# Kernel tuning notes

Measured on AMD Instinct MI355X. Metric: run time of the kernel, lower is better.

Reference implementation:

```python
import jax, jax.numpy as jnp
import numpy as np

DIM = 128
HEADS = 4


def setup_inputs() -> dict:
    key = jax.random.key(0)
    ks = jax.random.split(key, 6)
    B_, N, C = 2048, 49, DIM
    nW = 64
    x = jax.random.normal(ks[0], (B_, N, C), dtype=jnp.float32)
    mask = jax.random.normal(ks[1], (nW, N, N), dtype=jnp.float32)
    qkv_w = jax.random.normal(ks[2], (3 * C, C), dtype=jnp.float32) * 0.02
    qkv_b = jnp.zeros((3 * C,), dtype=jnp.float32)
    proj_w = jax.random.normal(ks[3], (C, C), dtype=jnp.float32) * 0.02
    proj_b = jnp.zeros((C,), dtype=jnp.float32)
    return {"x": x, "mask": mask, "qkv_w": qkv_w, "qkv_b": qkv_b,
            "proj_w": proj_w, "proj_b": proj_b}


def reference(x, mask, qkv_w, qkv_b, proj_w, proj_b):
    B_, N, C = x.shape
    H = HEADS
    Dh = C // H
    scale = Dh ** (-0.5)
    # fused QKV projection: [B_, N, 3C]
    qkv = x @ qkv_w.T + qkv_b
    qkv = qkv.reshape(B_, N, 3, H, Dh).transpose(2, 0, 3, 1, 4)  # [3, B_, H, N, Dh]
    q, k, v = qkv[0] * scale, qkv[1], qkv[2]
    attn = jnp.einsum('bhqd,bhkd->bhqk', q, k)  # [B_, H, N, N]
    nW = mask.shape[0]
    # add per-window additive mask: broadcast over images and heads
    attn = attn.reshape(B_ // nW, nW, H, N, N) + mask[None, :, None, :, :]
    attn = jax.nn.softmax(attn.reshape(B_, H, N, N), axis=-1)
    out = jnp.einsum('bhqk,bhkd->bhqd', attn, v)  # [B_, H, N, Dh]
    out = out.transpose(0, 2, 1, 3).reshape(B_, N, C)
    return out @ proj_w.T + proj_b
```

## Files before the change

kernel.cpp:

```cpp
#include <hip/hip_runtime.h>

typedef __bf16 bf16_t;
typedef __bf16 bf16x2 __attribute__((ext_vector_type(2)));
typedef __bf16 bf16x4 __attribute__((ext_vector_type(4)));
typedef __bf16 bf16x8 __attribute__((ext_vector_type(8)));
typedef float  f32x4  __attribute__((ext_vector_type(4)));
typedef float  f32x4u __attribute__((ext_vector_type(4), aligned(4)));
typedef unsigned int u32;

#define MFMA16(a, b, c) __builtin_amdgcn_mfma_f32_16x16x32_bf16((a), (b), (c), 0, 0, 0)

#define ROWB 272


union W8 { u32 u[4]; bf16x8 v; };

__device__ __forceinline__ u32 pack2(float a, float b) {
    union { bf16x2 h; u32 u; } c;
    c.h[0] = (bf16_t)a; c.h[1] = (bf16_t)b;
    return c.u;
}

__device__ __forceinline__ void st4(char* base, int row, int byteoff, bf16x4 v) {
    *(bf16x4*)(base + row * ROWB + byteoff) = v;
}
__device__ __forceinline__ bf16x8 ld8(const char* base, int row, int byteoff) {
    return *(const bf16x8*)(base + row * ROWB + byteoff);
}

__device__ __forceinline__ bf16x8 redist4(u32 w0, u32 w1, u32 w2, u32 w3,
                                          bool gl, bool gh) {
    u32 wd[4] = {w0, w1, w2, w3};
    u32 X[4], Y[4], Z[4];
    #pragma unroll
    for (int j = 0; j < 4; ++j) X[j] = __shfl_xor(wd[j], 16);
    #pragma unroll
    for (int j = 0; j < 4; ++j) Y[j] = __shfl_xor(wd[j], 32);
    #pragma unroll
    for (int j = 0; j < 4; ++j) Z[j] = __shfl_xor(X[j], 32);
    W8 u;
    #pragma unroll
    for (int t = 0; t < 4; ++t) {
        int j0 = t & 1;
        int j1 = j0 + 2;
        u32 lo, hi;
        if (t < 2) { lo = gl ? Z[j0] : wd[j0]; hi = gl ? X[j1] : Y[j1]; }
        else       { lo = gl ? Y[j0] : X[j0];  hi = gl ? wd[j1] : Z[j1]; }
        u.u[t] = gh ? hi : lo;
    }
    return u.v;
}

__global__ void wconv_kernel(const float* __restrict__ qw, const float* __restrict__ pw,
                             bf16_t* __restrict__ o) {
    int i = (blockIdx.x * 256 + threadIdx.x) * 4;
    const float* src = (i < 49152) ? (qw + i) : (pw + (i - 49152));
    float4 f = *(const float4*)src;
    bf16x4 h;
    h[0] = (bf16_t)f.x; h[1] = (bf16_t)f.y; h[2] = (bf16_t)f.z; h[3] = (bf16_t)f.w;
    *(bf16x4*)(o + i) = h;
}

template<int USEB>
__device__ __forceinline__ bf16x8 ldw(const float* __restrict__ wf,
                                      const bf16_t* __restrict__ wb, int idx) {
    if constexpr (USEB) {
        return *(const bf16x8*)(wb + idx);
    } else {
        float4 f0 = *(const float4*)(wf + idx);
        float4 f1 = *(const float4*)(wf + idx + 4);
        bf16x8 r;
        r[0] = (bf16_t)f0.x; r[1] = (bf16_t)f0.y; r[2] = (bf16_t)f0.z; r[3] = (bf16_t)f0.w;
        r[4] = (bf16_t)f1.x; r[5] = (bf16_t)f1.y; r[6] = (bf16_t)f1.z; r[7] = (bf16_t)f1.w;
        return r;
    }
}

template<int USEB>
__device__ __forceinline__ void pass_rowmajor(
    const char* xs, const float* __restrict__ wf, const bf16_t* __restrict__ wb,
    int rowbase, const float* __restrict__ biasp, float scale,
    int g, int c0, bool gl, bool gh, bf16x8 out[4])
{
    f32x4 acc[2][4];
    #pragma unroll
    for (int d = 0; d < 2; ++d)
        #pragma unroll
        for (int mt = 0; mt < 4; ++mt) acc[d][mt] = {0.f, 0.f, 0.f, 0.f};
    #pragma unroll
    for (int ks = 0; ks < 4; ++ks) {
        bf16x8 w0 = ldw<USEB>(wf, wb, (rowbase + c0) * 128 + 32 * ks + 8 * g);
        bf16x8 w1 = ldw<USEB>(wf, wb, (rowbase + 16 + c0) * 128 + 32 * ks + 8 * g);
        #pragma unroll
        for (int mt = 0; mt < 4; ++mt) {
            bf16x8 xf = ld8(xs, 16 * mt + c0, (32 * ks + 8 * g) * 2);
            acc[0][mt] = MFMA16(w0, xf, acc[0][mt]);
            acc[1][mt] = MFMA16(w1, xf, acc[1][mt]);
        }
    }
    float4 b0 = *(const float4*)(biasp + rowbase + 4 * g);
    float4 b1 = *(const float4*)(biasp + rowbase + 16 + 4 * g);
    #pragma unroll
    for (int t = 0; t < 4; ++t) {
        out[t] = redist4(
            pack2((acc[0][t][0] + b0.x) * scale, (acc[0][t][1] + b0.y) * scale),
            pack2((acc[0][t][2] + b0.z) * scale, (acc[0][t][3] + b0.w) * scale),
            pack2((acc[1][t][0] + b1.x) * scale, (acc[1][t][1] + b1.y) * scale),
            pack2((acc[1][t][2] + b1.z) * scale, (acc[1][t][3] + b1.w) * scale),
            gl, gh);
    }
}

template<int USEB>
__global__ __launch_bounds__(256, 4) void winattn_kernel(
    const float* __restrict__ xg, const float* __restrict__ maskg,
    const float* __restrict__ qwg, const float* __restrict__ qbg,
    const float* __restrict__ pwg, const float* __restrict__ pbg,
    const bf16_t* __restrict__ wqb, const bf16_t* __restrict__ wpb,
    const int nW, float* __restrict__ outg)
{
    __shared__ char xs[17408];

    const int b    = blockIdx.x;
    const int tid  = threadIdx.x;
    const int w    = tid >> 6;
    const int lane = tid & 63;
    const int g    = lane >> 4;
    const int c0   = lane & 15;
    const bool gl  = (g & 1) != 0, gh = (g & 2) != 0;
    const int h    = w;

    {
        const float4* xb = (const float4*)(xg + (long)b * 6272);
        #pragma unroll
        for (int it = 0; it < 7; ++it) {
            int i = tid + it * 256;
            if (i < 1568) {
                float4 f = xb[i];
                int row = i >> 5, colb = (i & 31) << 3;
                bf16x4 hq;
                hq[0] = (bf16_t)f.x; hq[1] = (bf16_t)f.y; hq[2] = (bf16_t)f.z; hq[3] = (bf16_t)f.w;
                st4(xs, row, colb, hq);
            }
        }
        #pragma unroll
        for (int it = 0; it < 4; ++it) {
            int i = tid + it * 256;
            if (i < 960) {
                int row = 49 + (i >> 6), byteo = (i & 63) << 2;
                *(u32*)(xs + row * ROWB + byteo) = 0u;
            }
        }
    }
    __syncthreads();

    const float qs = 0.17677669529663687f;
    bf16x8 qfr[4], ka[4];
    pass_rowmajor<USEB>(xs, qwg, wqb, 32 * h,       qbg, qs,  g, c0, gl, gh, qfr);
    pass_rowmajor<USEB>(xs, qwg, wqb, 128 + 32 * h, qbg, 1.f, g, c0, gl, gh, ka);

    bf16x8 va[2][2];
    {
        const int rb = 256 + 32 * h;
        f32x4 acc[4][2];
        #pragma unroll
        for (int mt = 0; mt < 4; ++mt)
            #pragma unroll
            for (int d = 0; d < 2; ++d) acc[mt][d] = {0.f, 0.f, 0.f, 0.f};
        #pragma unroll
        for (int ks = 0; ks < 4; ++ks) {
            bf16x8 w0 = ldw<USEB>(qwg, wqb, (rb + c0) * 128 + 32 * ks + 8 * g);
            bf16x8 w1 = ldw<USEB>(qwg, wqb, (rb + 16 + c0) * 128 + 32 * ks + 8 * g);
            #pragma unroll
            for (int mt = 0; mt < 4; ++mt) {
                bf16x8 xf = ld8(xs, 16 * mt + c0, (32 * ks + 8 * g) * 2);
                acc[mt][0] = MFMA16(xf, w0, acc[mt][0]);
                acc[mt][1] = MFMA16(xf, w1, acc[mt][1]);
            }
        }
        float vb0 = qbg[rb + c0];
        float vb1 = qbg[rb + 16 + c0];
        #pragma unroll
        for (int kt = 0; kt < 2; ++kt) {
            va[0][kt] = redist4(
                pack2(acc[2 * kt][0][0] + vb0, acc[2 * kt][0][1] + vb0),
                pack2(acc[2 * kt][0][2] + vb0, acc[2 * kt][0][3] + vb0),
                pack2(acc[2 * kt + 1][0][0] + vb0, acc[2 * kt + 1][0][1] + vb0),
                pack2(acc[2 * kt + 1][0][2] + vb0, acc[2 * kt + 1][0][3] + vb0),
                gl, gh);
            va[1][kt] = redist4(
                pack2(acc[2 * kt][1][0] + vb1, acc[2 * kt][1][1] + vb1),
                pack2(acc[2 * kt][1][2] + vb1, acc[2 * kt][1][3] + vb1),
                pack2(acc[2 * kt + 1][1][0] + vb1, acc[2 * kt + 1][1][1] + vb1),
                pack2(acc[2 * kt + 1][1][2] + vb1, acc[2 * kt + 1][1][3] + vb1),
                gl, gh);
        }
    }
    __syncthreads();

    const float* mrow = maskg + (long)(b % nW) * 2401;
    #pragma unroll
    for (int nt = 0; nt < 4; ++nt) {
        f32x4 s[4];
        #pragma unroll
        for (int kt = 0; kt < 4; ++kt) s[kt] = {0.f, 0.f, 0.f, 0.f};
        #pragma unroll
        for (int kt = 0; kt < 4; ++kt)
            s[kt] = MFMA16(ka[kt], qfr[nt], s[kt]);

        {
            int q  = 16 * nt + c0;
            int qm = q < 49 ? q : 48;
            const float* mr = mrow + qm * 49;
            f32x4u m0 = *(const f32x4u*)(mr + 4 * g);
            f32x4u m1 = *(const f32x4u*)(mr + 16 + 4 * g);
            f32x4u m2 = *(const f32x4u*)(mr + 32 + 4 * g);
            float m48 = mr[48];
            #pragma unroll
            for (int r = 0; r < 4; ++r) {
                s[0][r] += m0[r]; s[1][r] += m1[r]; s[2][r] += m2[r];
            }
            s[3][0] = (g == 0) ? s[3][0] + m48 : -1e30f;
            s[3][1] = -1e30f; s[3][2] = -1e30f; s[3][3] = -1e30f;
        }

        float mx = -1e30f;
        #pragma unroll
        for (int kt = 0; kt < 4; ++kt)
            #pragma unroll
            for (int r = 0; r < 4; ++r) mx = fmaxf(mx, s[kt][r]);
        mx = fmaxf(mx, __shfl_xor(mx, 16));
        mx = fmaxf(mx, __shfl_xor(mx, 32));

        float sum = 0.f;
        u32 wd[8];
        #pragma unroll
        for (int kt = 0; kt < 4; ++kt) {
            float e0 = __expf(s[kt][0] - mx), e1 = __expf(s[kt][1] - mx);
            float e2 = __expf(s[kt][2] - mx), e3 = __expf(s[kt][3] - mx);
            sum += (e0 + e1) + (e2 + e3);
            wd[2 * kt]     = pack2(e0, e1);
            wd[2 * kt + 1] = pack2(e2, e3);
        }
        sum += __shfl_xor(sum, 16);
        sum += __shfl_xor(sum, 32);
        float inv = 1.f / sum;

        bf16x8 pa0 = redist4(wd[0], wd[1], wd[2], wd[3], gl, gh);
        bf16x8 pa1 = redist4(wd[4], wd[5], wd[6], wd[7], gl, gh);

        f32x4 oo[2];
        oo[0] = {0.f, 0.f, 0.f, 0.f}; oo[1] = {0.f, 0.f, 0.f, 0.f};
        oo[0] = MFMA16(va[0][0], pa0, oo[0]);
        oo[0] = MFMA16(va[0][1], pa1, oo[0]);
        oo[1] = MFMA16(va[1][0], pa0, oo[1]);
        oo[1] = MFMA16(va[1][1], pa1, oo[1]);

        int q = 16 * nt + c0;
        #pragma unroll
        for (int dt = 0; dt < 2; ++dt) {
            bf16x4 t;
            t[0] = (bf16_t)(oo[dt][0] * inv); t[1] = (bf16_t)(oo[dt][1] * inv);
            t[2] = (bf16_t)(oo[dt][2] * inv); t[3] = (bf16_t)(oo[dt][3] * inv);
            st4(xs, q, (32 * h + 16 * dt + 4 * g) * 2, t);
        }
    }
    __syncthreads();

    {
        f32x4 acc[2][4];
        #pragma unroll
        for (int nt = 0; nt < 2; ++nt)
            #pragma unroll
            for (int mt = 0; mt < 4; ++mt) acc[nt][mt] = {0.f, 0.f, 0.f, 0.f};
        #pragma unroll
        for (int ks = 0; ks < 4; ++ks) {
            bf16x8 p0 = ldw<USEB>(pwg, wpb, (32 * w + c0) * 128 + 32 * ks + 8 * g);
            bf16x8 p1 = ldw<USEB>(pwg, wpb, (32 * w + 16 + c0) * 128 + 32 * ks + 8 * g);
            #pragma unroll
            for (int mt = 0; mt < 4; ++mt) {
                bf16x8 af = ld8(xs, 16 * mt + c0, (32 * ks + 8 * g) * 2);
                acc[0][mt] = MFMA16(p0, af, acc[0][mt]);
                acc[1][mt] = MFMA16(p1, af, acc[1][mt]);
            }
        }
        float4 pb0 = *(const float4*)(pbg + 32 * w + 4 * g);
        float4 pb1 = *(const float4*)(pbg + 32 * w + 16 + 4 * g);
        float* ob = outg + (long)b * 6272;
        #pragma unroll
        for (int nt = 0; nt < 2; ++nt) {
            float4 pb = nt ? pb1 : pb0;
            #pragma unroll
            for (int mt = 0; mt < 4; ++mt) {
                int tok = 16 * mt + c0;
                if (tok < 49) {
                    float4 t;
                    t.x = acc[nt][mt][0] + pb.x;
                    t.y = acc[nt][mt][1] + pb.y;
                    t.z = acc[nt][mt][2] + pb.z;
                    t.w = acc[nt][mt][3] + pb.w;
                    *(float4*)(ob + tok * 128 + 32 * w + 16 * nt + 4 * g) = t;
                }
            }
        }
    }
}

extern "C" void kernel_launch(void* const* d_in, const int* in_sizes, int n_in,
                              void* d_out, int out_size, void* d_ws, size_t ws_size,
                              hipStream_t stream) {
    const float* xg  = (const float*)d_in[0];
    const float* mg  = (const float*)d_in[1];
    const float* qwg = (const float*)d_in[2];
    const float* qbg = (const float*)d_in[3];
    const float* pwg = (const float*)d_in[4];
    const float* pbg = (const float*)d_in[5];
    float* outg = (float*)d_out;

    const int B  = in_sizes[0] / (49 * 128);
    const int nW = in_sizes[1] / (49 * 49);

    int use_wbf = (d_ws != nullptr && ws_size >= 131072) ? 1 : 0;
    bf16_t* wqb = (bf16_t*)d_ws;
    bf16_t* wpb = use_wbf ? (wqb + 49152) : nullptr;

    if (use_wbf) {
        wconv_kernel<<<64, 256, 0, stream>>>(qwg, pwg, wqb);
        winattn_kernel<1><<<B, 256, 0, stream>>>(
            xg, mg, qwg, qbg, pwg, pbg, wqb, wpb, nW, outg);
    } else {
        winattn_kernel<0><<<B, 256, 0, stream>>>(
            xg, mg, qwg, qbg, pwg, pbg, nullptr, nullptr, nW, outg);
    }
}
```

Baseline: 67.36 us.

## Load x fragments directly into registers, drop LDS staging and syncs

Each wave now reads its x rows straight from global memory into bf16 register fragments instead of staging the whole window through shared memory. This removes the LDS store/load round trip and two barriers. The projection weights and bias are also prefetched before the final barrier. In exchange every wave reloads all of x (four times the global/L2 traffic), register pressure rises, and launch bounds drop from four blocks per CU to three, reducing occupancy.

```diff
diff --git a/kernel.cpp b/kernel.cpp
--- a/kernel.cpp
+++ b/kernel.cpp
@@ -77,8 +77,8 @@
 }
 
 template<int USEB>
-__device__ __forceinline__ void pass_rowmajor(
-    const char* xs, const float* __restrict__ wf, const bf16_t* __restrict__ wb,
+__device__ __forceinline__ void qk_pass(
+    const bf16x8 xf[4][4], const float* __restrict__ wf, const bf16_t* __restrict__ wb,
     int rowbase, const float* __restrict__ biasp, float scale,
     int g, int c0, bool gl, bool gh, bf16x8 out[4])
 {
@@ -93,9 +93,8 @@
         bf16x8 w1 = ldw<USEB>(wf, wb, (rowbase + 16 + c0) * 128 + 32 * ks + 8 * g);
         #pragma unroll
         for (int mt = 0; mt < 4; ++mt) {
-            bf16x8 xf = ld8(xs, 16 * mt + c0, (32 * ks + 8 * g) * 2);
-            acc[0][mt] = MFMA16(w0, xf, acc[0][mt]);
-            acc[1][mt] = MFMA16(w1, xf, acc[1][mt]);
+            acc[0][mt] = MFMA16(w0, xf[mt][ks], acc[0][mt]);
+            acc[1][mt] = MFMA16(w1, xf[mt][ks], acc[1][mt]);
         }
     }
     float4 b0 = *(const float4*)(biasp + rowbase + 4 * g);
@@ -112,14 +111,14 @@
 }
 
 template<int USEB>
-__global__ __launch_bounds__(256, 4) void winattn_kernel(
+__global__ __launch_bounds__(256, 3) void winattn_kernel(
     const float* __restrict__ xg, const float* __restrict__ maskg,
     const float* __restrict__ qwg, const float* __restrict__ qbg,
     const float* __restrict__ pwg, const float* __restrict__ pbg,
     const bf16_t* __restrict__ wqb, const bf16_t* __restrict__ wpb,
     const int nW, float* __restrict__ outg)
 {
-    __shared__ char xs[17408];
+    __shared__ char as_[17408];
 
     const int b    = blockIdx.x;
     const int tid  = threadIdx.x;
@@ -130,34 +129,30 @@
     const bool gl  = (g & 1) != 0, gh = (g & 2) != 0;
     const int h    = w;
 
+    bf16x8 xf[4][4];
     {
-        const float4* xb = (const float4*)(xg + (long)b * 6272);
-        #pragma unroll
-        for (int it = 0; it < 7; ++it) {
-            int i = tid + it * 256;
-            if (i < 1568) {
-                float4 f = xb[i];
-                int row = i >> 5, colb = (i & 31) << 3;
-                bf16x4 hq;
-                hq[0] = (bf16_t)f.x; hq[1] = (bf16_t)f.y; hq[2] = (bf16_t)f.z; hq[3] = (bf16_t)f.w;
-                st4(xs, row, colb, hq);
-            }
-        }
-        #pragma unroll
-        for (int it = 0; it < 4; ++it) {
-            int i = tid + it * 256;
-            if (i < 960) {
-                int row = 49 + (i >> 6), byteo = (i & 63) << 2;
-                *(u32*)(xs + row * ROWB + byteo) = 0u;
-            }
-        }
-    }
-    __syncthreads();
+        const float* xb = xg + (long)b * 6272;
+        #pragma unroll
+        for (int mt = 0; mt < 4; ++mt) {
+            int row = 16 * mt + c0;
+            row = row > 48 ? 48 : row;
+            const float* rp = xb + row * 128 + 8 * g;
+            #pragma unroll
+            for (int ks = 0; ks < 4; ++ks) {
+                float4 f0 = *(const float4*)(rp + 32 * ks);
+                float4 f1 = *(const float4*)(rp + 32 * ks + 4);
+                bf16x8 r;
+                r[0] = (bf16_t)f0.x; r[1] = (bf16_t)f0.y; r[2] = (bf16_t)f0.z; r[3] = (bf16_t)f0.w;
+                r[4] = (bf16_t)f1.x; r[5] = (bf16_t)f1.y; r[6] = (bf16_t)f1.z; r[7] = (bf16_t)f1.w;
+                xf[mt][ks] = r;
+            }
+        }
+    }
 
     const float qs = 0.17677669529663687f;
     bf16x8 qfr[4], ka[4];
-    pass_rowmajor<USEB>(xs, qwg, wqb, 32 * h,       qbg, qs,  g, c0, gl, gh, qfr);
-    pass_rowmajor<USEB>(xs, qwg, wqb, 128 + 32 * h, qbg, 1.f, g, c0, gl, gh, ka);
+    qk_pass<USEB>(xf, qwg, wqb, 32 * h,       qbg, qs,  g, c0, gl, gh, qfr);
+    qk_pass<USEB>(xf, qwg, wqb, 128 + 32 * h, qbg, 1.f, g, c0, gl, gh, ka);
 
     bf16x8 va[2][2];
     {
@@ -173,9 +168,8 @@
             bf16x8 w1 = ldw<USEB>(qwg, wqb, (rb + 16 + c0) * 128 + 32 * ks + 8 * g);
             #pragma unroll
             for (int mt = 0; mt < 4; ++mt) {
-                bf16x8 xf = ld8(xs, 16 * mt + c0, (32 * ks + 8 * g) * 2);
-                acc[mt][0] = MFMA16(xf, w0, acc[mt][0]);
-                acc[mt][1] = MFMA16(xf, w1, acc[mt][1]);
+                acc[mt][0] = MFMA16(xf[mt][ks], w0, acc[mt][0]);
+                acc[mt][1] = MFMA16(xf[mt][ks], w1, acc[mt][1]);
             }
         }
         float vb0 = qbg[rb + c0];
@@ -196,7 +190,6 @@
                 gl, gh);
         }
     }
-    __syncthreads();
 
     const float* mrow = maskg + (long)(b % nW) * 2401;
     #pragma unroll
@@ -262,9 +255,18 @@
             bf16x4 t;
             t[0] = (bf16_t)(oo[dt][0] * inv); t[1] = (bf16_t)(oo[dt][1] * inv);
             t[2] = (bf16_t)(oo[dt][2] * inv); t[3] = (bf16_t)(oo[dt][3] * inv);
-            st4(xs, q, (32 * h + 16 * dt + 4 * g) * 2, t);
-        }
-    }
+            st4(as_, q, (32 * h + 16 * dt + 4 * g) * 2, t);
+        }
+    }
+
+    bf16x8 pwf[4][2];
+    #pragma unroll
+    for (int ks = 0; ks < 4; ++ks) {
+        pwf[ks][0] = ldw<USEB>(pwg, wpb, (32 * w + c0) * 128 + 32 * ks + 8 * g);
+        pwf[ks][1] = ldw<USEB>(pwg, wpb, (32 * w + 16 + c0) * 128 + 32 * ks + 8 * g);
+    }
+    float4 pb0 = *(const float4*)(pbg + 32 * w + 4 * g);
+    float4 pb1 = *(const float4*)(pbg + 32 * w + 16 + 4 * g);
     __syncthreads();
 
     {
@@ -275,17 +277,13 @@
             for (int mt = 0; mt < 4; ++mt) acc[nt][mt] = {0.f, 0.f, 0.f, 0.f};
         #pragma unroll
         for (int ks = 0; ks < 4; ++ks) {
-            bf16x8 p0 = ldw<USEB>(pwg, wpb, (32 * w + c0) * 128 + 32 * ks + 8 * g);
-            bf16x8 p1 = ldw<USEB>(pwg, wpb, (32 * w + 16 + c0) * 128 + 32 * ks + 8 * g);
             #pragma unroll
             for (int mt = 0; mt < 4; ++mt) {
-                bf16x8 af = ld8(xs, 16 * mt + c0, (32 * ks + 8 * g) * 2);
-                acc[0][mt] = MFMA16(p0, af, acc[0][mt]);
-                acc[1][mt] = MFMA16(p1, af, acc[1][mt]);
-            }
-        }
-        float4 pb0 = *(const float4*)(pbg + 32 * w + 4 * g);
-        float4 pb1 = *(const float4*)(pbg + 32 * w + 16 + 4 * g);
+                bf16x8 af = ld8(as_, 16 * mt + c0, (32 * ks + 8 * g) * 2);
+                acc[0][mt] = MFMA16(pwf[ks][0], af, acc[0][mt]);
+                acc[1][mt] = MFMA16(pwf[ks][1], af, acc[1][mt]);
+            }
+        }
         float* ob = outg + (long)b * 6272;
         #pragma unroll
         for (int nt = 0; nt < 2; ++nt) {
```

New measurement: 87.55 us. 30.0% more time.

## Split fused window attention into QKV projection and attention kernels

Applied to the files above, without the earlier changes.

Adds a two-kernel path: one kernel computes the QKV projection per window and writes bf16 Q/K/V to workspace in per-head layouts, and a second kernel reads them, runs masked softmax attention and the output projection. Each projection kernel spreads all 384 output channels across the four waves, which aims to balance MFMA work and cut the per-block register and serial-phase cost of the monolithic kernel. The split adds a round trip through global memory for Q/K/V (about 100 MB for B=2048) and one extra launch. It also hoists the projection weight loads before the barrier in both the fused and split attention paths.

```diff
diff --git a/kernel.cpp b/kernel.cpp
--- a/kernel.cpp
+++ b/kernel.cpp
@@ -76,8 +76,262 @@
     }
 }
 
+
 template<int USEB>
-__device__ __forceinline__ void pass_rowmajor(
+__global__ __launch_bounds__(256, 4) void qkv_kernel(
+    const float* __restrict__ xg, const float* __restrict__ qwg,
+    const float* __restrict__ qbg, const bf16_t* __restrict__ wqb,
+    bf16_t* __restrict__ qkv)
+{
+    __shared__ char xs[17408];
+    const int b    = blockIdx.x;
+    const int tid  = threadIdx.x;
+    const int w    = tid >> 6;
+    const int lane = tid & 63;
+    const int g    = lane >> 4;
+    const int c0   = lane & 15;
+
+    {
+        const float4* xb = (const float4*)(xg + (long)b * 6272);
+        #pragma unroll
+        for (int it = 0; it < 7; ++it) {
+            int i = tid + it * 256;
+            if (i < 1568) {
+                float4 f = xb[i];
+                int row = i >> 5, colb = (i & 31) << 3;
+                bf16x4 hq;
+                hq[0] = (bf16_t)f.x; hq[1] = (bf16_t)f.y; hq[2] = (bf16_t)f.z; hq[3] = (bf16_t)f.w;
+                st4(xs, row, colb, hq);
+            }
+        }
+        #pragma unroll
+        for (int it = 0; it < 4; ++it) {
+            int i = tid + it * 256;
+            if (i < 960) {
+                int row = 49 + (i >> 6), byteo = (i & 63) << 2;
+                *(u32*)(xs + row * ROWB + byteo) = 0u;
+            }
+        }
+    }
+    __syncthreads();
+
+    bf16_t* wb = qkv + (long)b * 24576;
+    const float qs = 0.17677669529663687f;
+
+    #pragma unroll
+    for (int half = 0; half < 2; ++half) {
+        f32x4 acc[3][4];
+        #pragma unroll
+        for (int t = 0; t < 3; ++t)
+            #pragma unroll
+            for (int mt = 0; mt < 4; ++mt) acc[t][mt] = {0.f, 0.f, 0.f, 0.f};
+
+        const int jb = 3 * half;
+        #pragma unroll
+        for (int ks = 0; ks < 4; ++ks) {
+            bf16x8 wf[3];
+            #pragma unroll
+            for (int t = 0; t < 3; ++t) {
+                int o0 = 96 * w + 16 * (jb + t);
+                wf[t] = ldw<USEB>(qwg, wqb, (o0 + c0) * 128 + 32 * ks + 8 * g);
+            }
+            #pragma unroll
+            for (int mt = 0; mt < 4; ++mt) {
+                bf16x8 xfm = ld8(xs, 16 * mt + c0, (32 * ks + 8 * g) * 2);
+                #pragma unroll
+                for (int t = 0; t < 3; ++t) {
+                    int o0 = 96 * w + 16 * (jb + t);
+                    if (o0 < 256) acc[t][mt] = MFMA16(wf[t], xfm, acc[t][mt]);
+                    else          acc[t][mt] = MFMA16(xfm, wf[t], acc[t][mt]);
+                }
+            }
+        }
+        #pragma unroll
+        for (int t = 0; t < 3; ++t) {
+            int o0   = 96 * w + 16 * (jb + t);
+            int part = o0 >> 7;
+            int hh   = (o0 >> 5) & 3;
+            bf16_t* hb = wb + hh * 6144;
+            if (part < 2) {
+                float4 b4 = *(const float4*)(qbg + o0 + 4 * g);
+                float sc  = (part == 0) ? qs : 1.f;
+                bf16_t* dst = hb + (part == 0 ? 0 : 2048);
+                int dh0 = (o0 & 31) + 4 * g;
+                #pragma unroll
+                for (int mt = 0; mt < 4; ++mt) {
+                    int tok = 16 * mt + c0;
+                    bf16x4 tv;
+                    tv[0] = (bf16_t)((acc[t][mt][0] + b4.x) * sc);
+                    tv[1] = (bf16_t)((acc[t][mt][1] + b4.y) * sc);
+                    tv[2] = (bf16_t)((acc[t][mt][2] + b4.z) * sc);
+                    tv[3] = (bf16_t)((acc[t][mt][3] + b4.w) * sc);
+                    *(bf16x4*)(dst + tok * 32 + dh0) = tv;
+                }
+            } else {
+                float bv = qbg[o0 + c0];
+                bf16_t* dst = hb + 4096;
+                int dh = (o0 & 31) + c0;
+                #pragma unroll
+                for (int mt = 0; mt < 4; ++mt) {
+                    bf16x4 tv;
+                    tv[0] = (bf16_t)(acc[t][mt][0] + bv);
+                    tv[1] = (bf16_t)(acc[t][mt][1] + bv);
+                    tv[2] = (bf16_t)(acc[t][mt][2] + bv);
+                    tv[3] = (bf16_t)(acc[t][mt][3] + bv);
+                    *(bf16x4*)(dst + dh * 64 + 16 * mt + 4 * g) = tv;
+                }
+            }
+        }
+    }
+}
+
+template<int USEB>
+__global__ __launch_bounds__(256, 4) void attn_kernel(
+    const bf16_t* __restrict__ qkv, const float* __restrict__ maskg,
+    const float* __restrict__ pwg, const float* __restrict__ pbg,
+    const bf16_t* __restrict__ wpb, const int nW, float* __restrict__ outg)
+{
+    __shared__ char as_[17408];
+
+    const int b    = blockIdx.x;
+    const int tid  = threadIdx.x;
+    const int w    = tid >> 6;
+    const int lane = tid & 63;
+    const int g    = lane >> 4;
+    const int c0   = lane & 15;
+    const bool gl  = (g & 1) != 0, gh = (g & 2) != 0;
+    const int h    = w;
+
+    const bf16_t* hb = qkv + (long)b * 24576 + h * 6144;
+    bf16x8 qfr[4], ka[4], va[2][2];
+    #pragma unroll
+    for (int t = 0; t < 4; ++t)
+        qfr[t] = *(const bf16x8*)(hb + (16 * t + c0) * 32 + 8 * g);
+    #pragma unroll
+    for (int kt = 0; kt < 4; ++kt)
+        ka[kt] = *(const bf16x8*)(hb + 2048 + (16 * kt + c0) * 32 + 8 * g);
+    #pragma unroll
+    for (int fi = 0; fi < 2; ++fi)
+        #pragma unroll
+        for (int kt = 0; kt < 2; ++kt)
+            va[fi][kt] = *(const bf16x8*)(hb + 4096 + (16 * fi + c0) * 64 + 32 * kt + 8 * g);
+
+    const float* mrow = maskg + (long)(b % nW) * 2401;
+    #pragma unroll
+    for (int nt = 0; nt < 4; ++nt) {
+        f32x4 s[4];
+        #pragma unroll
+        for (int kt = 0; kt < 4; ++kt) s[kt] = {0.f, 0.f, 0.f, 0.f};
+        #pragma unroll
+        for (int kt = 0; kt < 4; ++kt)
+            s[kt] = MFMA16(ka[kt], qfr[nt], s[kt]);
+
+        {
+            int q  = 16 * nt + c0;
+            int qm = q < 49 ? q : 48;
+            const float* mr = mrow + qm * 49;
+            f32x4u m0 = *(const f32x4u*)(mr + 4 * g);
+            f32x4u m1 = *(const f32x4u*)(mr + 16 + 4 * g);
+            f32x4u m2 = *(const f32x4u*)(mr + 32 + 4 * g);
+            float m48 = mr[48];
+            #pragma unroll
+            for (int r = 0; r < 4; ++r) {
+                s[0][r] += m0[r]; s[1][r] += m1[r]; s[2][r] += m2[r];
+            }
+            s[3][0] = (g == 0) ? s[3][0] + m48 : -1e30f;
+            s[3][1] = -1e30f; s[3][2] = -1e30f; s[3][3] = -1e30f;
+        }
+
+        float mx = -1e30f;
+        #pragma unroll
+        for (int kt = 0; kt < 4; ++kt)
+            #pragma unroll
+            for (int r = 0; r < 4; ++r) mx = fmaxf(mx, s[kt][r]);
+        mx = fmaxf(mx, __shfl_xor(mx, 16));
+        mx = fmaxf(mx, __shfl_xor(mx, 32));
+
+        float sum = 0.f;
+        u32 wd[8];
+        #pragma unroll
+        for (int kt = 0; kt < 4; ++kt) {
+            float e0 = __expf(s[kt][0] - mx), e1 = __expf(s[kt][1] - mx);
+            float e2 = __expf(s[kt][2] - mx), e3 = __expf(s[kt][3] - mx);
+            sum += (e0 + e1) + (e2 + e3);
+            wd[2 * kt]     = pack2(e0, e1);
+            wd[2 * kt + 1] = pack2(e2, e3);
+        }
+        sum += __shfl_xor(sum, 16);
+        sum += __shfl_xor(sum, 32);
+        float inv = 1.f / sum;
+
+        bf16x8 pa0 = redist4(wd[0], wd[1], wd[2], wd[3], gl, gh);
+        bf16x8 pa1 = redist4(wd[4], wd[5], wd[6], wd[7], gl, gh);
+
+        f32x4 oo[2];
+        oo[0] = {0.f, 0.f, 0.f, 0.f}; oo[1] = {0.f, 0.f, 0.f, 0.f};
+        oo[0] = MFMA16(va[0][0], pa0, oo[0]);
+        oo[0] = MFMA16(va[0][1], pa1, oo[0]);
+        oo[1] = MFMA16(va[1][0], pa0, oo[1]);
+        oo[1] = MFMA16(va[1][1], pa1, oo[1]);
+
+        int q = 16 * nt + c0;
+        #pragma unroll
+        for (int dt = 0; dt < 2; ++dt) {
+            bf16x4 t;
+            t[0] = (bf16_t)(oo[dt][0] * inv); t[1] = (bf16_t)(oo[dt][1] * inv);
+            t[2] = (bf16_t)(oo[dt][2] * inv); t[3] = (bf16_t)(oo[dt][3] * inv);
+            st4(as_, q, (32 * h + 16 * dt + 4 * g) * 2, t);
+        }
+    }
+
+    bf16x8 pwf[4][2];
+    #pragma unroll
+    for (int ks = 0; ks < 4; ++ks) {
+        pwf[ks][0] = ldw<USEB>(pwg, wpb, (32 * w + c0) * 128 + 32 * ks + 8 * g);
+        pwf[ks][1] = ldw<USEB>(pwg, wpb, (32 * w + 16 + c0) * 128 + 32 * ks + 8 * g);
+    }
+    float4 pb0 = *(const float4*)(pbg + 32 * w + 4 * g);
+    float4 pb1 = *(const float4*)(pbg + 32 * w + 16 + 4 * g);
+    __syncthreads();
+
+    {
+        f32x4 acc[2][4];
+        #pragma unroll
+        for (int nt = 0; nt < 2; ++nt)
+            #pragma unroll
+            for (int mt = 0; mt < 4; ++mt) acc[nt][mt] = {0.f, 0.f, 0.f, 0.f};
+        #pragma unroll
+        for (int ks = 0; ks < 4; ++ks) {
+            #pragma unroll
+            for (int mt = 0; mt < 4; ++mt) {
+                bf16x8 af = ld8(as_, 16 * mt + c0, (32 * ks + 8 * g) * 2);
+                acc[0][mt] = MFMA16(pwf[ks][0], af, acc[0][mt]);
+                acc[1][mt] = MFMA16(pwf[ks][1], af, acc[1][mt]);
+            }
+        }
+        float* ob = outg + (long)b * 6272;
+        #pragma unroll
+        for (int nt = 0; nt < 2; ++nt) {
+            float4 pb = nt ? pb1 : pb0;
+            #pragma unroll
+            for (int mt = 0; mt < 4; ++mt) {
+                int tok = 16 * mt + c0;
+                if (tok < 49) {
+                    float4 t;
+                    t.x = acc[nt][mt][0] + pb.x;
+                    t.y = acc[nt][mt][1] + pb.y;
+                    t.z = acc[nt][mt][2] + pb.z;
+                    t.w = acc[nt][mt][3] + pb.w;
+                    *(float4*)(ob + tok * 128 + 32 * w + 16 * nt + 4 * g) = t;
+                }
+            }
+        }
+    }
+}
+
+
+template<int USEB>
+__device__ __forceinline__ void qk_pass_f(
     const char* xs, const float* __restrict__ wf, const bf16_t* __restrict__ wb,
     int rowbase, const float* __restrict__ biasp, float scale,
     int g, int c0, bool gl, bool gh, bf16x8 out[4])
@@ -156,8 +410,8 @@
 
     const float qs = 0.17677669529663687f;
     bf16x8 qfr[4], ka[4];
-    pass_rowmajor<USEB>(xs, qwg, wqb, 32 * h,       qbg, qs,  g, c0, gl, gh, qfr);
-    pass_rowmajor<USEB>(xs, qwg, wqb, 128 + 32 * h, qbg, 1.f, g, c0, gl, gh, ka);
+    qk_pass_f<USEB>(xs, qwg, wqb, 32 * h,       qbg, qs,  g, c0, gl, gh, qfr);
+    qk_pass_f<USEB>(xs, qwg, wqb, 128 + 32 * h, qbg, 1.f, g, c0, gl, gh, ka);
 
     bf16x8 va[2][2];
     {
@@ -265,6 +519,15 @@
             st4(xs, q, (32 * h + 16 * dt + 4 * g) * 2, t);
         }
     }
+
+    bf16x8 pwf[4][2];
+    #pragma unroll
+    for (int ks = 0; ks < 4; ++ks) {
+        pwf[ks][0] = ldw<USEB>(pwg, wpb, (32 * w + c0) * 128 + 32 * ks + 8 * g);
+        pwf[ks][1] = ldw<USEB>(pwg, wpb, (32 * w + 16 + c0) * 128 + 32 * ks + 8 * g);
+    }
+    float4 pb0 = *(const float4*)(pbg + 32 * w + 4 * g);
+    float4 pb1 = *(const float4*)(pbg + 32 * w + 16 + 4 * g);
     __syncthreads();
 
     {
@@ -275,17 +538,13 @@
             for (int mt = 0; mt < 4; ++mt) acc[nt][mt] = {0.f, 0.f, 0.f, 0.f};
         #pragma unroll
         for (int ks = 0; ks < 4; ++ks) {
-            bf16x8 p0 = ldw<USEB>(pwg, wpb, (32 * w + c0) * 128 + 32 * ks + 8 * g);
-            bf16x8 p1 = ldw<USEB>(pwg, wpb, (32 * w + 16 + c0) * 128 + 32 * ks + 8 * g);
             #pragma unroll
             for (int mt = 0; mt < 4; ++mt) {
                 bf16x8 af = ld8(xs, 16 * mt + c0, (32 * ks + 8 * g) * 2);
-                acc[0][mt] = MFMA16(p0, af, acc[0][mt]);
-                acc[1][mt] = MFMA16(p1, af, acc[1][mt]);
-            }
-        }
-        float4 pb0 = *(const float4*)(pbg + 32 * w + 4 * g);
-        float4 pb1 = *(const float4*)(pbg + 32 * w + 16 + 4 * g);
+                acc[0][mt] = MFMA16(pwf[ks][0], af, acc[0][mt]);
+                acc[1][mt] = MFMA16(pwf[ks][1], af, acc[1][mt]);
+            }
+        }
         float* ob = outg + (long)b * 6272;
         #pragma unroll
         for (int nt = 0; nt < 2; ++nt) {
@@ -320,11 +579,19 @@
     const int B  = in_sizes[0] / (49 * 128);
     const int nW = in_sizes[1] / (49 * 49);
 
-    int use_wbf = (d_ws != nullptr && ws_size >= 131072) ? 1 : 0;
-    bf16_t* wqb = (bf16_t*)d_ws;
-    bf16_t* wpb = use_wbf ? (wqb + 49152) : nullptr;
-
-    if (use_wbf) {
+    const size_t QKV_EL    = (size_t)B * 24576;
+    const size_t NEED_SPLIT = QKV_EL * 2 + 131072;
+
+    if (d_ws != nullptr && ws_size >= NEED_SPLIT) {
+        bf16_t* qkvws = (bf16_t*)d_ws;
+        bf16_t* wqb   = qkvws + QKV_EL;
+        bf16_t* wpb   = wqb + 49152;
+        wconv_kernel<<<64, 256, 0, stream>>>(qwg, pwg, wqb);
+        qkv_kernel<1><<<B, 256, 0, stream>>>(xg, qwg, qbg, wqb, qkvws);
+        attn_kernel<1><<<B, 256, 0, stream>>>(qkvws, mg, pwg, pbg, wpb, nW, outg);
+    } else if (d_ws != nullptr && ws_size >= 131072) {
+        bf16_t* wqb = (bf16_t*)d_ws;
+        bf16_t* wpb = wqb + 49152;
         wconv_kernel<<<64, 256, 0, stream>>>(qwg, pwg, wqb);
         winattn_kernel<1><<<B, 256, 0, stream>>>(
             xg, mg, qwg, qbg, pwg, pbg, wqb, wpb, nW, outg);
```

Result: slower. 129.9 us (+92.8%).

## Persistent multi-window blocks with register-resident QKV weights and x prefetch

Applied to the files above, without the earlier changes.

Replaces the one-window-per-block kernel with a persistent 512-thread kernel where each of 512 blocks handles B/512 windows in sequence. Each wave keeps its QK weight fragments in registers across windows, and the work is split among 8 waves, with Q/K/V staged in dynamic shared memory per head. The next window's x is prefetched into registers during attention. The goal is to avoid reloading weights per window and to hide global load latency, at the cost of more barriers per window, 75KB of LDS, and only 512 blocks for occupancy.

```diff
diff --git a/kernel.cpp b/kernel.cpp
--- a/kernel.cpp
+++ b/kernel.cpp
@@ -26,6 +26,11 @@
 }
 __device__ __forceinline__ bf16x8 ld8(const char* base, int row, int byteoff) {
     return *(const bf16x8*)(base + row * ROWB + byteoff);
+}
+__device__ __forceinline__ void stx(char* buf, int i, float4 f) {
+    bf16x4 hq;
+    hq[0] = (bf16_t)f.x; hq[1] = (bf16_t)f.y; hq[2] = (bf16_t)f.z; hq[3] = (bf16_t)f.w;
+    st4(buf, i >> 5, (i & 31) << 3, hq);
 }
 
 __device__ __forceinline__ bf16x8 redist4(u32 w0, u32 w1, u32 w2, u32 w3,
@@ -61,24 +66,253 @@
     *(bf16x4*)(o + i) = h;
 }
 
-template<int USEB>
-__device__ __forceinline__ bf16x8 ldw(const float* __restrict__ wf,
-                                      const bf16_t* __restrict__ wb, int idx) {
-    if constexpr (USEB) {
-        return *(const bf16x8*)(wb + idx);
-    } else {
-        float4 f0 = *(const float4*)(wf + idx);
-        float4 f1 = *(const float4*)(wf + idx + 4);
-        bf16x8 r;
-        r[0] = (bf16_t)f0.x; r[1] = (bf16_t)f0.y; r[2] = (bf16_t)f0.z; r[3] = (bf16_t)f0.w;
-        r[4] = (bf16_t)f1.x; r[5] = (bf16_t)f1.y; r[6] = (bf16_t)f1.z; r[7] = (bf16_t)f1.w;
-        return r;
-    }
-}
-
-template<int USEB>
-__device__ __forceinline__ void pass_rowmajor(
-    const char* xs, const float* __restrict__ wf, const bf16_t* __restrict__ wb,
+__global__ __launch_bounds__(512, 4) void mwin_kernel(
+    const float* __restrict__ xg, const float* __restrict__ maskg,
+    const bf16_t* __restrict__ wqb, const float* __restrict__ qbg,
+    const bf16_t* __restrict__ wpb, const float* __restrict__ pbg,
+    const int nW, const int WPB, const int Btot, float* __restrict__ outg)
+{
+    extern __shared__ char smem[];
+    char*   xbuf  = smem;
+    bf16_t* heads = (bf16_t*)(smem + 17408);
+
+    const int tid  = threadIdx.x;
+    const int w    = tid >> 6;
+    const int lane = tid & 63;
+    const int g    = lane >> 4;
+    const int c0   = lane & 15;
+    const bool gl  = (g & 1) != 0, gh = (g & 2) != 0;
+    const float qs = 0.17677669529663687f;
+
+    const int oqk = 32 * w;
+    bf16x8 wqk[2][4];
+    #pragma unroll
+    for (int nt = 0; nt < 2; ++nt)
+        #pragma unroll
+        for (int ks = 0; ks < 4; ++ks)
+            wqk[nt][ks] = *(const bf16x8*)(wqb + (oqk + 16*nt + c0)*128 + 32*ks + 8*g);
+    float4 bqk[2];
+    bqk[0] = *(const float4*)(qbg + oqk + 4*g);
+    bqk[1] = *(const float4*)(qbg + oqk + 16 + 4*g);
+    const int   ov   = 256 + 16 * w;
+    const float bv   = qbg[ov + c0];
+    const float qmul = (w < 4) ? qs : 1.f;
+
+    bf16_t* qkdst = heads + (w & 3) * 7424 + (w < 4 ? 0 : 2560);
+    bf16_t* vdst  = heads + (w >> 1) * 7424 + 5120 + (16*(w & 1) + c0) * 72;
+
+    const int h = w >> 1, qh2 = w & 1;
+    const bf16_t* qls = heads + h * 7424;
+    const bf16_t* kls = qls + 2560;
+    const bf16_t* vls = qls + 5120;
+
+    const long b0 = (long)blockIdx.x * WPB;
+    if (b0 >= Btot) return;
+
+    for (int i = tid; i < 960; i += 512) {
+        int row = 49 + (i >> 6), byteo = (i & 63) << 2;
+        *(u32*)(xbuf + row * ROWB + byteo) = 0u;
+    }
+    {
+        const float4* xb = (const float4*)(xg + b0 * 6272);
+        float4 f0 = xb[tid], f1 = xb[tid + 512], f2 = xb[tid + 1024];
+        stx(xbuf, tid, f0); stx(xbuf, tid + 512, f1); stx(xbuf, tid + 1024, f2);
+        if (tid < 32) { float4 f3 = xb[tid + 1536]; stx(xbuf, tid + 1536, f3); }
+    }
+    __syncthreads();
+
+    for (int j = 0; j < WPB; ++j) {
+        const long b = b0 + j;
+
+        {
+            f32x4 aqk[2][4];
+            #pragma unroll
+            for (int nt = 0; nt < 2; ++nt)
+                #pragma unroll
+                for (int mt = 0; mt < 4; ++mt) aqk[nt][mt] = {0.f, 0.f, 0.f, 0.f};
+            #pragma unroll
+            for (int ks = 0; ks < 4; ++ks)
+                #pragma unroll
+                for (int mt = 0; mt < 4; ++mt) {
+                    bf16x8 xf = ld8(xbuf, 16*mt + c0, (32*ks + 8*g) * 2);
+                    aqk[0][mt] = MFMA16(wqk[0][ks], xf, aqk[0][mt]);
+                    aqk[1][mt] = MFMA16(wqk[1][ks], xf, aqk[1][mt]);
+                }
+            #pragma unroll
+            for (int nt = 0; nt < 2; ++nt) {
+                int dh0 = 16*nt + 4*g;
+                #pragma unroll
+                for (int mt = 0; mt < 4; ++mt) {
+                    int tok = 16*mt + c0;
+                    bf16x4 tv;
+                    tv[0] = (bf16_t)((aqk[nt][mt][0] + bqk[nt].x) * qmul);
+                    tv[1] = (bf16_t)((aqk[nt][mt][1] + bqk[nt].y) * qmul);
+                    tv[2] = (bf16_t)((aqk[nt][mt][2] + bqk[nt].z) * qmul);
+                    tv[3] = (bf16_t)((aqk[nt][mt][3] + bqk[nt].w) * qmul);
+                    *(bf16x4*)(qkdst + tok*40 + dh0) = tv;
+                }
+            }
+            f32x4 av[4];
+            #pragma unroll
+            for (int mt = 0; mt < 4; ++mt) av[mt] = {0.f, 0.f, 0.f, 0.f};
+            #pragma unroll
+            for (int ks = 0; ks < 4; ++ks) {
+                bf16x8 wvk = *(const bf16x8*)(wqb + (ov + c0)*128 + 32*ks + 8*g);
+                #pragma unroll
+                for (int mt = 0; mt < 4; ++mt) {
+                    bf16x8 xf = ld8(xbuf, 16*mt + c0, (32*ks + 8*g) * 2);
+                    av[mt] = MFMA16(xf, wvk, av[mt]);
+                }
+            }
+            #pragma unroll
+            for (int mt = 0; mt < 4; ++mt) {
+                bf16x4 tv;
+                tv[0] = (bf16_t)(av[mt][0] + bv);
+                tv[1] = (bf16_t)(av[mt][1] + bv);
+                tv[2] = (bf16_t)(av[mt][2] + bv);
+                tv[3] = (bf16_t)(av[mt][3] + bv);
+                *(bf16x4*)(vdst + 16*mt + 4*g) = tv;
+            }
+        }
+        __syncthreads();
+
+        float4 xr0, xr1, xr2, xr3;
+        const bool pre = (j + 1 < WPB);
+        if (pre) {
+            const float4* xn = (const float4*)(xg + (b + 1) * 6272);
+            xr0 = xn[tid]; xr1 = xn[tid + 512]; xr2 = xn[tid + 1024];
+            if (tid < 32) xr3 = xn[tid + 1536];
+        }
+        {
+            bf16x8 ka[4], qb2[2], va[2][2];
+            #pragma unroll
+            for (int kt = 0; kt < 4; ++kt)
+                ka[kt] = *(const bf16x8*)(kls + (16*kt + c0)*40 + 8*g);
+            #pragma unroll
+            for (int nt = 0; nt < 2; ++nt)
+                qb2[nt] = *(const bf16x8*)(qls + ((2*qh2 + nt)*16 + c0)*40 + 8*g);
+            #pragma unroll
+            for (int fi = 0; fi < 2; ++fi)
+                #pragma unroll
+                for (int kt = 0; kt < 2; ++kt)
+                    va[fi][kt] = *(const bf16x8*)(vls + (16*fi + c0)*72 + 32*kt + 8*g);
+
+            const float* mrow = maskg + (long)(b % nW) * 2401;
+            #pragma unroll
+            for (int nt = 0; nt < 2; ++nt) {
+                f32x4 s[4];
+                #pragma unroll
+                for (int kt = 0; kt < 4; ++kt) s[kt] = {0.f, 0.f, 0.f, 0.f};
+                #pragma unroll
+                for (int kt = 0; kt < 4; ++kt)
+                    s[kt] = MFMA16(ka[kt], qb2[nt], s[kt]);
+
+                int q  = (2*qh2 + nt)*16 + c0;
+                int qm = q < 49 ? q : 48;
+                const float* mr = mrow + qm * 49;
+                f32x4u m0 = *(const f32x4u*)(mr + 4*g);
+                f32x4u m1 = *(const f32x4u*)(mr + 16 + 4*g);
+                f32x4u m2 = *(const f32x4u*)(mr + 32 + 4*g);
+                float m48 = mr[48];
+                #pragma unroll
+                for (int r = 0; r < 4; ++r) {
+                    s[0][r] += m0[r]; s[1][r] += m1[r]; s[2][r] += m2[r];
+                }
+                s[3][0] = (g == 0) ? s[3][0] + m48 : -1e30f;
+                s[3][1] = -1e30f; s[3][2] = -1e30f; s[3][3] = -1e30f;
+
+                float mx = -1e30f;
+                #pragma unroll
+                for (int kt = 0; kt < 4; ++kt)
+                    #pragma unroll
+                    for (int r = 0; r < 4; ++r) mx = fmaxf(mx, s[kt][r]);
+                mx = fmaxf(mx, __shfl_xor(mx, 16));
+                mx = fmaxf(mx, __shfl_xor(mx, 32));
+
+                float sum = 0.f;
+                u32 wd[8];
+                #pragma unroll
+                for (int kt = 0; kt < 4; ++kt) {
+                    float e0 = __expf(s[kt][0] - mx), e1 = __expf(s[kt][1] - mx);
+                    float e2 = __expf(s[kt][2] - mx), e3 = __expf(s[kt][3] - mx);
+                    sum += (e0 + e1) + (e2 + e3);
+                    wd[2*kt]     = pack2(e0, e1);
+                    wd[2*kt + 1] = pack2(e2, e3);
+                }
+                sum += __shfl_xor(sum, 16);
+                sum += __shfl_xor(sum, 32);
+                float inv = 1.f / sum;
+
+                bf16x8 pa0 = redist4(wd[0], wd[1], wd[2], wd[3], gl, gh);
+                bf16x8 pa1 = redist4(wd[4], wd[5], wd[6], wd[7], gl, gh);
+
+                f32x4 oo0 = {0.f, 0.f, 0.f, 0.f}, oo1 = {0.f, 0.f, 0.f, 0.f};
+                oo0 = MFMA16(va[0][0], pa0, oo0);
+                oo0 = MFMA16(va[0][1], pa1, oo0);
+                oo1 = MFMA16(va[1][0], pa0, oo1);
+                oo1 = MFMA16(va[1][1], pa1, oo1);
+
+                bf16x4 t0, t1;
+                t0[0] = (bf16_t)(oo0[0] * inv); t0[1] = (bf16_t)(oo0[1] * inv);
+                t0[2] = (bf16_t)(oo0[2] * inv); t0[3] = (bf16_t)(oo0[3] * inv);
+                t1[0] = (bf16_t)(oo1[0] * inv); t1[1] = (bf16_t)(oo1[1] * inv);
+                t1[2] = (bf16_t)(oo1[2] * inv); t1[3] = (bf16_t)(oo1[3] * inv);
+                st4(xbuf, q, (32*h + 4*g) * 2, t0);
+                st4(xbuf, q, (32*h + 16 + 4*g) * 2, t1);
+            }
+        }
+        __syncthreads();
+
+        {
+            bf16x8 pwf[4];
+            #pragma unroll
+            for (int ks = 0; ks < 4; ++ks)
+                pwf[ks] = *(const bf16x8*)(wpb + (16*w + c0)*128 + 32*ks + 8*g);
+            float4 pb4 = *(const float4*)(pbg + 16*w + 4*g);
+            f32x4 pacc[4];
+            #pragma unroll
+            for (int mt = 0; mt < 4; ++mt) pacc[mt] = {0.f, 0.f, 0.f, 0.f};
+            #pragma unroll
+            for (int ks = 0; ks < 4; ++ks)
+                #pragma unroll
+                for (int mt = 0; mt < 4; ++mt) {
+                    bf16x8 af = ld8(xbuf, 16*mt + c0, (32*ks + 8*g) * 2);
+                    pacc[mt] = MFMA16(pwf[ks], af, pacc[mt]);
+                }
+            float* ob = outg + b * 6272;
+            #pragma unroll
+            for (int mt = 0; mt < 4; ++mt) {
+                int tok = 16*mt + c0;
+                if (tok < 49) {
+                    float4 t;
+                    t.x = pacc[mt][0] + pb4.x;
+                    t.y = pacc[mt][1] + pb4.y;
+                    t.z = pacc[mt][2] + pb4.z;
+                    t.w = pacc[mt][3] + pb4.w;
+                    *(float4*)(ob + tok*128 + 16*w + 4*g) = t;
+                }
+            }
+        }
+        if (pre) {
+            __syncthreads();
+            stx(xbuf, tid, xr0); stx(xbuf, tid + 512, xr1); stx(xbuf, tid + 1024, xr2);
+            if (tid < 32) stx(xbuf, tid + 1536, xr3);
+            __syncthreads();
+        }
+    }
+}
+
+__device__ __forceinline__ bf16x8 ldwf(const float* __restrict__ wf, int idx) {
+    float4 f0 = *(const float4*)(wf + idx);
+    float4 f1 = *(const float4*)(wf + idx + 4);
+    bf16x8 r;
+    r[0] = (bf16_t)f0.x; r[1] = (bf16_t)f0.y; r[2] = (bf16_t)f0.z; r[3] = (bf16_t)f0.w;
+    r[4] = (bf16_t)f1.x; r[5] = (bf16_t)f1.y; r[6] = (bf16_t)f1.z; r[7] = (bf16_t)f1.w;
+    return r;
+}
+
+__device__ __forceinline__ void qk_pass_f(
+    const char* xs, const float* __restrict__ wf,
     int rowbase, const float* __restrict__ biasp, float scale,
     int g, int c0, bool gl, bool gh, bf16x8 out[4])
 {
@@ -89,17 +323,17 @@
         for (int mt = 0; mt < 4; ++mt) acc[d][mt] = {0.f, 0.f, 0.f, 0.f};
     #pragma unroll
     for (int ks = 0; ks < 4; ++ks) {
-        bf16x8 w0 = ldw<USEB>(wf, wb, (rowbase + c0) * 128 + 32 * ks + 8 * g);
-        bf16x8 w1 = ldw<USEB>(wf, wb, (rowbase + 16 + c0) * 128 + 32 * ks + 8 * g);
+        bf16x8 w0 = ldwf(wf, (rowbase + c0) * 128 + 32*ks + 8*g);
+        bf16x8 w1 = ldwf(wf, (rowbase + 16 + c0) * 128 + 32*ks + 8*g);
         #pragma unroll
         for (int mt = 0; mt < 4; ++mt) {
-            bf16x8 xf = ld8(xs, 16 * mt + c0, (32 * ks + 8 * g) * 2);
+            bf16x8 xf = ld8(xs, 16*mt + c0, (32*ks + 8*g) * 2);
             acc[0][mt] = MFMA16(w0, xf, acc[0][mt]);
             acc[1][mt] = MFMA16(w1, xf, acc[1][mt]);
         }
     }
-    float4 b0 = *(const float4*)(biasp + rowbase + 4 * g);
-    float4 b1 = *(const float4*)(biasp + rowbase + 16 + 4 * g);
+    float4 b0 = *(const float4*)(biasp + rowbase + 4*g);
+    float4 b1 = *(const float4*)(biasp + rowbase + 16 + 4*g);
     #pragma unroll
     for (int t = 0; t < 4; ++t) {
         out[t] = redist4(
@@ -111,16 +345,13 @@
     }
 }
 
-template<int USEB>
-__global__ __launch_bounds__(256, 4) void winattn_kernel(
+__global__ __launch_bounds__(256, 4) void winattn_fb(
     const float* __restrict__ xg, const float* __restrict__ maskg,
     const float* __restrict__ qwg, const float* __restrict__ qbg,
     const float* __restrict__ pwg, const float* __restrict__ pbg,
-    const bf16_t* __restrict__ wqb, const bf16_t* __restrict__ wpb,
     const int nW, float* __restrict__ outg)
 {
     __shared__ char xs[17408];
-
     const int b    = blockIdx.x;
     const int tid  = threadIdx.x;
     const int w    = tid >> 6;
@@ -135,13 +366,7 @@
         #pragma unroll
         for (int it = 0; it < 7; ++it) {
             int i = tid + it * 256;
-            if (i < 1568) {
-                float4 f = xb[i];
-                int row = i >> 5, colb = (i & 31) << 3;
-                bf16x4 hq;
-                hq[0] = (bf16_t)f.x; hq[1] = (bf16_t)f.y; hq[2] = (bf16_t)f.z; hq[3] = (bf16_t)f.w;
-                st4(xs, row, colb, hq);
-            }
+            if (i < 1568) { float4 f = xb[i]; stx(xs, i, f); }
         }
         #pragma unroll
         for (int it = 0; it < 4; ++it) {
@@ -156,12 +381,12 @@
 
     const float qs = 0.17677669529663687f;
     bf16x8 qfr[4], ka[4];
-    pass_rowmajor<USEB>(xs, qwg, wqb, 32 * h,       qbg, qs,  g, c0, gl, gh, qfr);
-    pass_rowmajor<USEB>(xs, qwg, wqb, 128 + 32 * h, qbg, 1.f, g, c0, gl, gh, ka);
+    qk_pass_f(xs, qwg, 32*h,       qbg, qs,  g, c0, gl, gh, qfr);
+    qk_pass_f(xs, qwg, 128 + 32*h, qbg, 1.f, g, c0, gl, gh, ka);
 
     bf16x8 va[2][2];
     {
-        const int rb = 256 + 32 * h;
+        const int rb = 256 + 32*h;
         f32x4 acc[4][2];
         #pragma unroll
         for (int mt = 0; mt < 4; ++mt)
@@ -169,11 +394,11 @@
             for (int d = 0; d < 2; ++d) acc[mt][d] = {0.f, 0.f, 0.f, 0.f};
         #pragma unroll
         for (int ks = 0; ks < 4; ++ks) {
-            bf16x8 w0 = ldw<USEB>(qwg, wqb, (rb + c0) * 128 + 32 * ks + 8 * g);
-            bf16x8 w1 = ldw<USEB>(qwg, wqb, (rb + 16 + c0) * 128 + 32 * ks + 8 * g);
+            bf16x8 w0 = ldwf(qwg, (rb + c0) * 128 + 32*ks + 8*g);
+            bf16x8 w1 = ldwf(qwg, (rb + 16 + c0) * 128 + 32*ks + 8*g);
             #pragma unroll
             for (int mt = 0; mt < 4; ++mt) {
-                bf16x8 xf = ld8(xs, 16 * mt + c0, (32 * ks + 8 * g) * 2);
+                bf16x8 xf = ld8(xs, 16*mt + c0, (32*ks + 8*g) * 2);
                 acc[mt][0] = MFMA16(xf, w0, acc[mt][0]);
                 acc[mt][1] = MFMA16(xf, w1, acc[mt][1]);
             }
@@ -183,16 +408,16 @@
         #pragma unroll
         for (int kt = 0; kt < 2; ++kt) {
             va[0][kt] = redist4(
-                pack2(acc[2 * kt][0][0] + vb0, acc[2 * kt][0][1] + vb0),
-                pack2(acc[2 * kt][0][2] + vb0, acc[2 * kt][0][3] + vb0),
-                pack2(acc[2 * kt + 1][0][0] + vb0, acc[2 * kt + 1][0][1] + vb0),
-                pack2(acc[2 * kt + 1][0][2] + vb0, acc[2 * kt + 1][0][3] + vb0),
+                pack2(acc[2*kt][0][0] + vb0, acc[2*kt][0][1] + vb0),
+                pack2(acc[2*kt][0][2] + vb0, acc[2*kt][0][3] + vb0),
+                pack2(acc[2*kt+1][0][0] + vb0, acc[2*kt+1][0][1] + vb0),
+                pack2(acc[2*kt+1][0][2] + vb0, acc[2*kt+1][0][3] + vb0),
                 gl, gh);
             va[1][kt] = redist4(
-                pack2(acc[2 * kt][1][0] + vb1, acc[2 * kt][1][1] + vb1),
-                pack2(acc[2 * kt][1][2] + vb1, acc[2 * kt][1][3] + vb1),
-                pack2(acc[2 * kt + 1][1][0] + vb1, acc[2 * kt + 1][1][1] + vb1),
-                pack2(acc[2 * kt + 1][1][2] + vb1, acc[2 * kt + 1][1][3] + vb1),
+                pack2(acc[2*kt][1][0] + vb1, acc[2*kt][1][1] + vb1),
+                pack2(acc[2*kt][1][2] + vb1, acc[2*kt][1][3] + vb1),
+                pack2(acc[2*kt+1][1][0] + vb1, acc[2*kt+1][1][1] + vb1),
+                pack2(acc[2*kt+1][1][2] + vb1, acc[2*kt+1][1][3] + vb1),
                 gl, gh);
         }
     }
@@ -207,14 +432,13 @@
         #pragma unroll
         for (int kt = 0; kt < 4; ++kt)
             s[kt] = MFMA16(ka[kt], qfr[nt], s[kt]);
-
         {
-            int q  = 16 * nt + c0;
+            int q  = 16*nt + c0;
             int qm = q < 49 ? q : 48;
             const float* mr = mrow + qm * 49;
-            f32x4u m0 = *(const f32x4u*)(mr + 4 * g);
-            f32x4u m1 = *(const f32x4u*)(mr + 16 + 4 * g);
-            f32x4u m2 = *(const f32x4u*)(mr + 32 + 4 * g);
+            f32x4u m0 = *(const f32x4u*)(mr + 4*g);
+            f32x4u m1 = *(const f32x4u*)(mr + 16 + 4*g);
+            f32x4u m2 = *(const f32x4u*)(mr + 32 + 4*g);
             float m48 = mr[48];
             #pragma unroll
             for (int r = 0; r < 4; ++r) {
@@ -223,7 +447,6 @@
             s[3][0] = (g == 0) ? s[3][0] + m48 : -1e30f;
             s[3][1] = -1e30f; s[3][2] = -1e30f; s[3][3] = -1e30f;
         }
-
         float mx = -1e30f;
         #pragma unroll
         for (int kt = 0; kt < 4; ++kt)
@@ -231,7 +454,6 @@
             for (int r = 0; r < 4; ++r) mx = fmaxf(mx, s[kt][r]);
         mx = fmaxf(mx, __shfl_xor(mx, 16));
         mx = fmaxf(mx, __shfl_xor(mx, 32));
-
         float sum = 0.f;
         u32 wd[8];
         #pragma unroll
@@ -239,8 +461,8 @@
             float e0 = __expf(s[kt][0] - mx), e1 = __expf(s[kt][1] - mx);
             float e2 = __expf(s[kt][2] - mx), e3 = __expf(s[kt][3] - mx);
             sum += (e0 + e1) + (e2 + e3);
-            wd[2 * kt]     = pack2(e0, e1);
-            wd[2 * kt + 1] = pack2(e2, e3);
+            wd[2*kt]     = pack2(e0, e1);
+            wd[2*kt + 1] = pack2(e2, e3);
         }
         sum += __shfl_xor(sum, 16);
         sum += __shfl_xor(sum, 32);
@@ -256,15 +478,24 @@
         oo[1] = MFMA16(va[1][0], pa0, oo[1]);
         oo[1] = MFMA16(va[1][1], pa1, oo[1]);
 
-        int q = 16 * nt + c0;
+        int q = 16*nt + c0;
         #pragma unroll
         for (int dt = 0; dt < 2; ++dt) {
             bf16x4 t;
             t[0] = (bf16_t)(oo[dt][0] * inv); t[1] = (bf16_t)(oo[dt][1] * inv);
             t[2] = (bf16_t)(oo[dt][2] * inv); t[3] = (bf16_t)(oo[dt][3] * inv);
-            st4(xs, q, (32 * h + 16 * dt + 4 * g) * 2, t);
-        }
-    }
+            st4(xs, q, (32*h + 16*dt + 4*g) * 2, t);
+        }
+    }
+
+    bf16x8 pwf[4][2];
+    #pragma unroll
+    for (int ks = 0; ks < 4; ++ks) {
+        pwf[ks][0] = ldwf(pwg, (32*w + c0) * 128 + 32*ks + 8*g);
+        pwf[ks][1] = ldwf(pwg, (32*w + 16 + c0) * 128 + 32*ks + 8*g);
+    }
+    float4 pb0 = *(const float4*)(pbg + 32*w + 4*g);
+    float4 pb1 = *(const float4*)(pbg + 32*w + 16 + 4*g);
     __syncthreads();
 
     {
@@ -275,31 +506,27 @@
             for (int mt = 0; mt < 4; ++mt) acc[nt][mt] = {0.f, 0.f, 0.f, 0.f};
         #pragma unroll
         for (int ks = 0; ks < 4; ++ks) {
-            bf16x8 p0 = ldw<USEB>(pwg, wpb, (32 * w + c0) * 128 + 32 * ks + 8 * g);
-            bf16x8 p1 = ldw<USEB>(pwg, wpb, (32 * w + 16 + c0) * 128 + 32 * ks + 8 * g);
             #pragma unroll
             for (int mt = 0; mt < 4; ++mt) {
-                bf16x8 af = ld8(xs, 16 * mt + c0, (32 * ks + 8 * g) * 2);
-                acc[0][mt] = MFMA16(p0, af, acc[0][mt]);
-                acc[1][mt] = MFMA16(p1, af, acc[1][mt]);
-            }
-        }
-        float4 pb0 = *(const float4*)(pbg + 32 * w + 4 * g);
-        float4 pb1 = *(const float4*)(pbg + 32 * w + 16 + 4 * g);
+                bf16x8 af = ld8(xs, 16*mt + c0, (32*ks + 8*g) * 2);
+                acc[0][mt] = MFMA16(pwf[ks][0], af, acc[0][mt]);
+                acc[1][mt] = MFMA16(pwf[ks][1], af, acc[1][mt]);
+            }
+        }
         float* ob = outg + (long)b * 6272;
         #pragma unroll
         for (int nt = 0; nt < 2; ++nt) {
             float4 pb = nt ? pb1 : pb0;
             #pragma unroll
             for (int mt = 0; mt < 4; ++mt) {
-                int tok = 16 * mt + c0;
+                int tok = 16*mt + c0;
                 if (tok < 49) {
                     float4 t;
                     t.x = acc[nt][mt][0] + pb.x;
                     t.y = acc[nt][mt][1] + pb.y;
                     t.z = acc[nt][mt][2] + pb.z;
                     t.w = acc[nt][mt][3] + pb.w;
-                    *(float4*)(ob + tok * 128 + 32 * w + 16 * nt + 4 * g) = t;
+                    *(float4*)(ob + tok*128 + 32*w + 16*nt + 4*g) = t;
                 }
             }
         }
@@ -320,16 +547,18 @@
     const int B  = in_sizes[0] / (49 * 128);
     const int nW = in_sizes[1] / (49 * 49);
 
-    int use_wbf = (d_ws != nullptr && ws_size >= 131072) ? 1 : 0;
-    bf16_t* wqb = (bf16_t*)d_ws;
-    bf16_t* wpb = use_wbf ? (wqb + 49152) : nullptr;
-
-    if (use_wbf) {
+    const int NBLK = 512;
+    if (d_ws != nullptr && ws_size >= 131072 && (B % NBLK) == 0) {
+        bf16_t* wqb = (bf16_t*)d_ws;
+        bf16_t* wpb = wqb + 49152;
         wconv_kernel<<<64, 256, 0, stream>>>(qwg, pwg, wqb);
-        winattn_kernel<1><<<B, 256, 0, stream>>>(
-            xg, mg, qwg, qbg, pwg, pbg, wqb, wpb, nW, outg);
+        (void)hipFuncSetAttribute((const void*)mwin_kernel,
+                                  hipFuncAttributeMaxDynamicSharedMemorySize, 76800);
+        const int WPB = B / NBLK;
+        mwin_kernel<<<NBLK, 512, 76800, stream>>>(
+            xg, mg, wqb, qbg, wpb, pbg, nW, WPB, B, outg);
     } else {
-        winattn_kernel<0><<<B, 256, 0, stream>>>(
-            xg, mg, qwg, qbg, pwg, pbg, nullptr, nullptr, nW, outg);
-    }
-}
+        winattn_fb<<<B, 256, 0, stream>>>(
+            xg, mg, qwg, qbg, pwg, pbg, nW, outg);
+    }
+}
```

Result: slower. 93.34 us (+38.6%).
